# Kernel optimization log

Hardware: AMD Instinct MI355X
Metric: run time of the kernel (lower is better)

Reference implementation:

```python
import jax, jax.numpy as jnp
import numpy as np

ATOM_FDIM = 35
BOND_FDIM = 5
MAX_NB = 15
HIDDEN = 512
DEPTH = 6
N_MOLS = 1024
ATOMS_PER_MOL = 32
N_ATOMS = N_MOLS * ATOMS_PER_MOL      # 32768
N_BONDS = 2 * N_ATOMS                  # 65536 (each bond appears in both directions)
N_MESS = 8192                          # tree messages (row 0 is the zero pad slot)
TOTAL_MSG = N_MESS + N_BONDS           # index space for agraph/bgraph


def setup_inputs() -> dict:
    key = jax.random.key(0)
    ks = jax.random.split(key, 8)
    fatoms = jax.random.normal(ks[0], (N_ATOMS, ATOM_FDIM), jnp.float32)
    fbonds = jax.random.normal(ks[1], (N_BONDS, ATOM_FDIM + BOND_FDIM), jnp.float32)
    agraph = jax.random.randint(ks[2], (N_ATOMS, MAX_NB), 0, TOTAL_MSG, dtype=jnp.int32)
    bgraph = jax.random.randint(ks[3], (N_BONDS, MAX_NB), 0, TOTAL_MSG, dtype=jnp.int32)
    # row 0 of the concatenated message table is the padding slot -> zero it
    tree_message = jax.random.normal(ks[4], (N_MESS, HIDDEN), jnp.float32).at[0].set(0.0)
    starts = jnp.arange(N_MOLS, dtype=jnp.int32) * ATOMS_PER_MOL
    scope = jnp.stack([starts, jnp.full((N_MOLS,), ATOMS_PER_MOL, jnp.int32)], axis=1)
    s_i = 1.0 / np.sqrt(ATOM_FDIM + BOND_FDIM)
    s_h = 1.0 / np.sqrt(HIDDEN)
    s_o = 1.0 / np.sqrt(ATOM_FDIM + HIDDEN)
    W_i = jax.random.normal(ks[5], (ATOM_FDIM + BOND_FDIM, HIDDEN), jnp.float32) * s_i
    W_h = jax.random.normal(ks[6], (HIDDEN, HIDDEN), jnp.float32) * s_h
    W_o = jax.random.normal(ks[7], (ATOM_FDIM + HIDDEN, HIDDEN), jnp.float32) * s_o
    b_o = jnp.zeros((HIDDEN,), jnp.float32)
    return {"fatoms": fatoms, "fbonds": fbonds, "agraph": agraph, "bgraph": bgraph,
            "scope": scope, "tree_message": tree_message,
            "W_i": W_i, "W_h": W_h, "W_o": W_o, "b_o": b_o}


def reference(fatoms, fbonds, agraph, bgraph, scope, tree_message, W_i, W_h, W_o, b_o):
    binput = fbonds @ W_i                         # [B, H]
    graph_message = jax.nn.relu(binput)

    def step(gm, _):
        message = jnp.concatenate([tree_message, gm], axis=0)   # [M+B, H]
        nei = message[bgraph].sum(axis=1)                       # gather-sum [B, H]
        return jax.nn.relu(binput + nei @ W_h), None

    graph_message, _ = jax.lax.scan(step, graph_message, None, length=DEPTH - 1)

    message = jnp.concatenate([tree_message, graph_message], axis=0)
    nei = message[agraph].sum(axis=1)             # [A, H]
    ainput = jnp.concatenate([fatoms, nei], axis=1)
    atom_hiddens = jax.nn.relu(ainput @ W_o + b_o)

    # scope is uniform (st = i*ATOMS_PER_MOL, le = ATOMS_PER_MOL) -> static segment ids
    seg = jnp.repeat(jnp.arange(N_MOLS), ATOMS_PER_MOL)
    sums = jax.ops.segment_sum(atom_hiddens, seg, num_segments=N_MOLS)
    return sums / scope[:, 1:].astype(atom_hiddens.dtype)
```

## Files before the change

### kernel.cpp

```cpp
#include <hip/hip_runtime.h>
#include <stdint.h>


#define MAX_NB 15
#define HID 512
#define NA 32768
#define NB 65536
#define NMESS 8192

typedef unsigned short u16;
typedef unsigned int u32;
typedef __bf16 bf16x8 __attribute__((ext_vector_type(8)));
typedef float f32x4 __attribute__((ext_vector_type(4)));

__device__ __forceinline__ u16 f2bf(float f) {
  u32 u = __builtin_bit_cast(u32, f);
  u32 r = (u + 0x7fffu + ((u >> 16) & 1u)) >> 16;
  return (u16)r;
}
__device__ __forceinline__ float bf2f(u16 b) {
  u32 u = ((u32)b) << 16;
  return __builtin_bit_cast(float, u);
}
__device__ __forceinline__ float bflo(u32 u) {
  return __builtin_bit_cast(float, u << 16);
}
__device__ __forceinline__ float bfhi(u32 u) {
  return __builtin_bit_cast(float, u & 0xffff0000u);
}

__device__ __forceinline__ void async16(const u16* g, u16* l) {
  __builtin_amdgcn_global_load_lds(
      (const __attribute__((address_space(1))) u32*)g,
      (__attribute__((address_space(3))) u32*)l, 16, 0, 0);
}

__global__ __launch_bounds__(256) void prep_kernel(
    const float* __restrict__ fbonds, const float* __restrict__ tree,
    const float* __restrict__ Wi, const float* __restrict__ Wh,
    const float* __restrict__ Wo, u16* __restrict__ tree_bf,
    u16* __restrict__ fbpad, u16* __restrict__ wi_t, u16* __restrict__ wh_t,
    u16* __restrict__ wo_t) {
  int t = blockIdx.x * 256 + threadIdx.x;
  const int N0 = NMESS * HID;
  const int N1 = NB * 64;
  const int N2 = 512 * 64;
  const int N3 = 512 * 512;
  const int N4 = 512 * 576;
  if (t < N0) { tree_bf[t] = f2bf(tree[t]); return; }
  t -= N0;
  if (t < N1) {
    int row = t >> 6, c = t & 63;
    fbpad[t] = (c < 40) ? f2bf(fbonds[row * 40 + c]) : (u16)0;
    return;
  }
  t -= N1;
  if (t < N2) {
    int n = t >> 6, k = t & 63;
    wi_t[t] = (k < 40) ? f2bf(Wi[k * 512 + n]) : (u16)0;
    return;
  }
  t -= N2;
  if (t < N3) {
    int n = t >> 9, k = t & 511;
    wh_t[t] = f2bf(Wh[k * 512 + n]);
    return;
  }
  t -= N3;
  if (t < N4) {
    int n = t / 576, k = t - n * 576;
    float v = 0.f;
    if (k < 512) v = Wo[(35 + k) * 512 + n];
    else if (k < 547) v = Wo[(k - 512) * 512 + n];
    wo_t[t] = f2bf(v);
    return;
  }
}

__global__ __launch_bounds__(256) void init_gemm(
    const u16* __restrict__ A, const u16* __restrict__ Bt,
    u16* __restrict__ binput, u16* __restrict__ gm0) {
  const int K = 64;
  __shared__ __align__(16) u16 As[128 * 32];
  __shared__ __align__(16) u16 Bs[128 * 32];
  const int t = threadIdx.x;
  const int lane = t & 63;
  const int w = t >> 6;
  const int wm = w & 1, wn = w >> 1;
  const int mBase = blockIdx.x * 128;
  const int nBase = blockIdx.y * 128;
  const int r = t >> 2;
  const int c8 = (t & 3) * 8;
  const int q8 = (lane >> 4) * 8;
  const int l15 = lane & 15;

  f32x4 acc[4][4];
#pragma unroll
  for (int i = 0; i < 4; i++)
#pragma unroll
    for (int j = 0; j < 4; j++)
#pragma unroll
      for (int rg = 0; rg < 4; rg++) acc[i][j][rg] = 0.f;

  for (int kb = 0; kb < K; kb += 32) {
    __syncthreads();
    async16(A + (size_t)(mBase + r) * K + kb + c8, As + r * 32 + c8);
    async16(A + (size_t)(mBase + r + 64) * K + kb + c8, As + (r + 64) * 32 + c8);
    async16(Bt + (size_t)(nBase + r) * K + kb + c8, Bs + r * 32 + c8);
    async16(Bt + (size_t)(nBase + r + 64) * K + kb + c8, Bs + (r + 64) * 32 + c8);
    __syncthreads();
    bf16x8 av[4], bv[4];
#pragma unroll
    for (int i = 0; i < 4; i++)
      av[i] = *(const bf16x8*)(As + (wm * 64 + i * 16 + l15) * 32 + q8);
#pragma unroll
    for (int j = 0; j < 4; j++)
      bv[j] = *(const bf16x8*)(Bs + (wn * 64 + j * 16 + l15) * 32 + q8);
#pragma unroll
    for (int i = 0; i < 4; i++)
#pragma unroll
      for (int j = 0; j < 4; j++)
        acc[i][j] = __builtin_amdgcn_mfma_f32_16x16x32_bf16(av[i], bv[j],
                                                            acc[i][j], 0, 0, 0);
  }
#pragma unroll
  for (int i = 0; i < 4; i++) {
    int row = mBase + wm * 64 + i * 16 + (lane >> 4) * 4;
#pragma unroll
    for (int j = 0; j < 4; j++) {
      int col = nBase + wn * 64 + j * 16 + l15;
#pragma unroll
      for (int rg = 0; rg < 4; rg++) {
        float v = acc[i][j][rg];
        size_t gi = (size_t)(row + rg) * HID + col;
        binput[gi] = f2bf(v);
        gm0[gi] = f2bf(fmaxf(v, 0.f));
      }
    }
  }
}

template <int OUT>
__global__ __launch_bounds__(512, 4) void fused_step(
    const u16* __restrict__ tree, const u16* __restrict__ gm_prev,
    const int* __restrict__ graph, const u16* __restrict__ Bt,
    const u16* __restrict__ binput, u16* __restrict__ gm_next,
    const float* __restrict__ fatoms, const float* __restrict__ bo,
    const int* __restrict__ scope, float* __restrict__ out) {
  const int K = OUT ? 576 : 512;
  const int NCH = K / 64;
  __shared__ __align__(16) u16 As[64 * 72];
  const int t = threadIdx.x;
  const int lane = t & 63;
  const int w = t >> 6;
  const int l15 = lane & 15;
  const int q8 = (lane >> 4) * 8;
  const int mBase = blockIdx.x * 64;
  const int slot = t >> 3;
  const int sub = t & 7;

  f32x4 acc[4][4];
#pragma unroll
  for (int i = 0; i < 4; i++)
#pragma unroll
    for (int j = 0; j < 4; j++)
#pragma unroll
      for (int rg = 0; rg < 4; rg++) acc[i][j][rg] = 0.f;

  const int* idx = graph + (size_t)(mBase + slot) * MAX_NB;
  const u16* gm_sh = gm_prev - (size_t)NMESS * HID;

  for (int ch = 0; ch < NCH; ch++) {
    const int kb = ch * 64;
    __syncthreads();
    float g[8] = {0.f, 0.f, 0.f, 0.f, 0.f, 0.f, 0.f, 0.f};
    if (OUT && ch == NCH - 1) {
#pragma unroll
      for (int e = 0; e < 8; e++) {
        int c = sub * 8 + e;
        g[e] = (c < 35) ? fatoms[(size_t)(mBase + slot) * 35 + c] : 0.f;
      }
    } else {
#pragma unroll
      for (int j = 0; j < MAX_NB; j++) {
        int id = idx[j];
        const u16* base = (id < NMESS) ? tree : gm_sh;
        uint4 v = *(const uint4*)(base + (size_t)id * HID + kb + sub * 8);
        g[0] += bflo(v.x); g[1] += bfhi(v.x);
        g[2] += bflo(v.y); g[3] += bfhi(v.y);
        g[4] += bflo(v.z); g[5] += bfhi(v.z);
        g[6] += bflo(v.w); g[7] += bfhi(v.w);
      }
    }
    uint4 o;
    o.x = (u32)f2bf(g[0]) | ((u32)f2bf(g[1]) << 16);
    o.y = (u32)f2bf(g[2]) | ((u32)f2bf(g[3]) << 16);
    o.z = (u32)f2bf(g[4]) | ((u32)f2bf(g[5]) << 16);
    o.w = (u32)f2bf(g[6]) | ((u32)f2bf(g[7]) << 16);
    *(uint4*)(As + slot * 72 + sub * 8) = o;
    __syncthreads();
#pragma unroll
    for (int s = 0; s < 2; s++) {
      bf16x8 av[4], bv[4];
#pragma unroll
      for (int i = 0; i < 4; i++)
        av[i] = *(const bf16x8*)(As + (i * 16 + l15) * 72 + s * 32 + q8);
#pragma unroll
      for (int j = 0; j < 4; j++)
        bv[j] = *(const bf16x8*)(Bt + (size_t)(w * 64 + j * 16 + l15) * K + kb +
                                 s * 32 + q8);
#pragma unroll
      for (int i = 0; i < 4; i++)
#pragma unroll
        for (int j = 0; j < 4; j++)
          acc[i][j] = __builtin_amdgcn_mfma_f32_16x16x32_bf16(
              av[i], bv[j], acc[i][j], 0, 0, 0);
    }
  }

  if (OUT) {
#pragma unroll
    for (int m = 0; m < 2; m++) {
      int mol = (mBase >> 5) + m;
      float inv_le = 1.0f / (float)scope[mol * 2 + 1];
#pragma unroll
      for (int j = 0; j < 4; j++) {
        int col = w * 64 + j * 16 + l15;
        float bias = bo[col];
        float s = 0.f;
#pragma unroll
        for (int i = 2 * m; i < 2 * m + 2; i++)
#pragma unroll
          for (int rg = 0; rg < 4; rg++)
            s += fmaxf(acc[i][j][rg] + bias, 0.f);
        s += __shfl_xor(s, 16, 64);
        s += __shfl_xor(s, 32, 64);
        if (lane < 16) out[(size_t)mol * HID + col] = s * inv_le;
      }
    }
  } else {
#pragma unroll
    for (int i = 0; i < 4; i++) {
      int row = mBase + i * 16 + (lane >> 4) * 4;
#pragma unroll
      for (int j = 0; j < 4; j++) {
        int col = w * 64 + j * 16 + l15;
#pragma unroll
        for (int rg = 0; rg < 4; rg++) {
          size_t gi = (size_t)(row + rg) * HID + col;
          float v = acc[i][j][rg] + bf2f(binput[gi]);
          gm_next[gi] = f2bf(fmaxf(v, 0.f));
        }
      }
    }
  }
}

extern "C" void kernel_launch(void* const* d_in, const int* in_sizes, int n_in,
                              void* d_out, int out_size, void* d_ws,
                              size_t ws_size, hipStream_t stream) {
  const float* fatoms = (const float*)d_in[0];
  const float* fbonds = (const float*)d_in[1];
  const int* agraph = (const int*)d_in[2];
  const int* bgraph = (const int*)d_in[3];
  const int* scope = (const int*)d_in[4];
  const float* tree = (const float*)d_in[5];
  const float* Wi = (const float*)d_in[6];
  const float* Wh = (const float*)d_in[7];
  const float* Wo = (const float*)d_in[8];
  const float* bo = (const float*)d_in[9];
  float* out = (float*)d_out;

  char* ws = (char*)d_ws;
  u16* tree_bf = (u16*)(ws);
  u16* gmA = (u16*)(ws + 8388608ull);
  u16* gmB = (u16*)(ws + 75497472ull);
  u16* binput = (u16*)(ws + 142606336ull);
  u16* wi_t = (u16*)(ws + 209715200ull);
  u16* wh_t = (u16*)(ws + 209780736ull);
  u16* wo_t = (u16*)(ws + 210305024ull);
  u16* fbpad = gmB;

  prep_kernel<<<35072, 256, 0, stream>>>(fbonds, tree, Wi, Wh, Wo, tree_bf,
                                         fbpad, wi_t, wh_t, wo_t);

  init_gemm<<<dim3(NB / 128, 4), 256, 0, stream>>>(fbpad, wi_t, binput, gmA);

  u16* prev = gmA;
  u16* next = gmB;
  for (int d = 0; d < 5; d++) {
    fused_step<0><<<NB / 64, 512, 0, stream>>>(tree_bf, prev, bgraph, wh_t,
                                               binput, next, nullptr, nullptr,
                                               nullptr, nullptr);
    u16* tmp = prev; prev = next; next = tmp;
  }

  fused_step<1><<<NA / 64, 512, 0, stream>>>(tree_bf, prev, agraph, wo_t,
                                             nullptr, nullptr, fatoms, bo,
                                             scope, out);
}
```

Before: 1.335 ms.

## Gather full neighbor-sum rows into LDS once, then run the whole K loop

```diff
diff --git a/kernel.cpp b/kernel.cpp
--- a/kernel.cpp
+++ b/kernel.cpp
@@ -141,81 +141,72 @@
 }
 
 template <int OUT>
-__global__ __launch_bounds__(512, 4) void fused_step(
+__global__ __launch_bounds__(512, 4) void fused_mp(
     const u16* __restrict__ tree, const u16* __restrict__ gm_prev,
     const int* __restrict__ graph, const u16* __restrict__ Bt,
     const u16* __restrict__ binput, u16* __restrict__ gm_next,
     const float* __restrict__ fatoms, const float* __restrict__ bo,
     const int* __restrict__ scope, float* __restrict__ out) {
-  const int K = OUT ? 576 : 512;
-  const int NCH = K / 64;
-  __shared__ __align__(16) u16 As[64 * 72];
+  constexpr int K = OUT ? 576 : 512;
+  constexpr int LDA = K + 8;
+  __shared__ __align__(16) u16 As[64 * LDA];
   const int t = threadIdx.x;
   const int lane = t & 63;
   const int w = t >> 6;
+  const int mBase = blockIdx.x * 64;
+  const u16* gm_sh = gm_prev - (size_t)NMESS * HID;
+
+  for (int rr = 0; rr < 8; rr++) {
+    const int row = mBase + w * 8 + rr;
+    const int* idxp = graph + row * MAX_NB;
+    float acc[8] = {0, 0, 0, 0, 0, 0, 0, 0};
+#pragma unroll
+    for (int j = 0; j < MAX_NB; j++) {
+      int id = idxp[j];
+      const u16* base = (id < NMESS) ? tree : gm_sh;
+      uint4 v = *(const uint4*)(base + (size_t)id * HID + lane * 8);
+      acc[0] += bflo(v.x); acc[1] += bfhi(v.x);
+      acc[2] += bflo(v.y); acc[3] += bfhi(v.y);
+      acc[4] += bflo(v.z); acc[5] += bfhi(v.z);
+      acc[6] += bflo(v.w); acc[7] += bfhi(v.w);
+    }
+    uint4 o;
+    o.x = (u32)f2bf(acc[0]) | ((u32)f2bf(acc[1]) << 16);
+    o.y = (u32)f2bf(acc[2]) | ((u32)f2bf(acc[3]) << 16);
+    o.z = (u32)f2bf(acc[4]) | ((u32)f2bf(acc[5]) << 16);
+    o.w = (u32)f2bf(acc[6]) | ((u32)f2bf(acc[7]) << 16);
+    *(uint4*)(As + (w * 8 + rr) * LDA + lane * 8) = o;
+    if (OUT) {
+      float tv = (lane < 35) ? fatoms[(size_t)row * 35 + lane] : 0.f;
+      As[(w * 8 + rr) * LDA + 512 + lane] = f2bf(tv);
+    }
+  }
+  __syncthreads();
+
   const int l15 = lane & 15;
   const int q8 = (lane >> 4) * 8;
-  const int mBase = blockIdx.x * 64;
-  const int slot = t >> 3;
-  const int sub = t & 7;
-
-  f32x4 acc[4][4];
+  f32x4 acc2[4][4];
 #pragma unroll
   for (int i = 0; i < 4; i++)
 #pragma unroll
     for (int j = 0; j < 4; j++)
 #pragma unroll
-      for (int rg = 0; rg < 4; rg++) acc[i][j][rg] = 0.f;
-
-  const int* idx = graph + (size_t)(mBase + slot) * MAX_NB;
-  const u16* gm_sh = gm_prev - (size_t)NMESS * HID;
-
-  for (int ch = 0; ch < NCH; ch++) {
-    const int kb = ch * 64;
-    __syncthreads();
-    float g[8] = {0.f, 0.f, 0.f, 0.f, 0.f, 0.f, 0.f, 0.f};
-    if (OUT && ch == NCH - 1) {
-#pragma unroll
-      for (int e = 0; e < 8; e++) {
-        int c = sub * 8 + e;
-        g[e] = (c < 35) ? fatoms[(size_t)(mBase + slot) * 35 + c] : 0.f;
-      }
-    } else {
-#pragma unroll
-      for (int j = 0; j < MAX_NB; j++) {
-        int id = idx[j];
-        const u16* base = (id < NMESS) ? tree : gm_sh;
-        uint4 v = *(const uint4*)(base + (size_t)id * HID + kb + sub * 8);
-        g[0] += bflo(v.x); g[1] += bfhi(v.x);
-        g[2] += bflo(v.y); g[3] += bfhi(v.y);
-        g[4] += bflo(v.z); g[5] += bfhi(v.z);
-        g[6] += bflo(v.w); g[7] += bfhi(v.w);
-      }
-    }
-    uint4 o;
-    o.x = (u32)f2bf(g[0]) | ((u32)f2bf(g[1]) << 16);
-    o.y = (u32)f2bf(g[2]) | ((u32)f2bf(g[3]) << 16);
-    o.z = (u32)f2bf(g[4]) | ((u32)f2bf(g[5]) << 16);
-    o.w = (u32)f2bf(g[6]) | ((u32)f2bf(g[7]) << 16);
-    *(uint4*)(As + slot * 72 + sub * 8) = o;
-    __syncthreads();
-#pragma unroll
-    for (int s = 0; s < 2; s++) {
-      bf16x8 av[4], bv[4];
-#pragma unroll
-      for (int i = 0; i < 4; i++)
-        av[i] = *(const bf16x8*)(As + (i * 16 + l15) * 72 + s * 32 + q8);
+      for (int rg = 0; rg < 4; rg++) acc2[i][j][rg] = 0.f;
+
+  for (int kb = 0; kb < K; kb += 32) {
+    bf16x8 av[4], bv[4];
+#pragma unroll
+    for (int i = 0; i < 4; i++)
+      av[i] = *(const bf16x8*)(As + (i * 16 + l15) * LDA + kb + q8);
+#pragma unroll
+    for (int j = 0; j < 4; j++)
+      bv[j] = *(const bf16x8*)(Bt + (size_t)(w * 64 + j * 16 + l15) * K + kb + q8);
+#pragma unroll
+    for (int i = 0; i < 4; i++)
 #pragma unroll
       for (int j = 0; j < 4; j++)
-        bv[j] = *(const bf16x8*)(Bt + (size_t)(w * 64 + j * 16 + l15) * K + kb +
-                                 s * 32 + q8);
-#pragma unroll
-      for (int i = 0; i < 4; i++)
-#pragma unroll
-        for (int j = 0; j < 4; j++)
-          acc[i][j] = __builtin_amdgcn_mfma_f32_16x16x32_bf16(
-              av[i], bv[j], acc[i][j], 0, 0, 0);
-    }
+        acc2[i][j] = __builtin_amdgcn_mfma_f32_16x16x32_bf16(av[i], bv[j],
+                                                             acc2[i][j], 0, 0, 0);
   }
 
   if (OUT) {
@@ -232,7 +223,7 @@
         for (int i = 2 * m; i < 2 * m + 2; i++)
 #pragma unroll
           for (int rg = 0; rg < 4; rg++)
-            s += fmaxf(acc[i][j][rg] + bias, 0.f);
+            s += fmaxf(acc2[i][j][rg] + bias, 0.f);
         s += __shfl_xor(s, 16, 64);
         s += __shfl_xor(s, 32, 64);
         if (lane < 16) out[(size_t)mol * HID + col] = s * inv_le;
@@ -248,7 +239,7 @@
 #pragma unroll
         for (int rg = 0; rg < 4; rg++) {
           size_t gi = (size_t)(row + rg) * HID + col;
-          float v = acc[i][j][rg] + bf2f(binput[gi]);
+          float v = acc2[i][j][rg] + bf2f(binput[gi]);
           gm_next[gi] = f2bf(fmaxf(v, 0.f));
         }
       }
@@ -289,13 +280,13 @@
   u16* prev = gmA;
   u16* next = gmB;
   for (int d = 0; d < 5; d++) {
-    fused_step<0><<<NB / 64, 512, 0, stream>>>(tree_bf, prev, bgraph, wh_t,
-                                               binput, next, nullptr, nullptr,
-                                               nullptr, nullptr);
+    fused_mp<0><<<NB / 64, 512, 0, stream>>>(tree_bf, prev, bgraph, wh_t,
+                                             binput, next, nullptr, nullptr,
+                                             nullptr, nullptr);
     u16* tmp = prev; prev = next; next = tmp;
   }
 
-  fused_step<1><<<NA / 64, 512, 0, stream>>>(tree_bf, prev, agraph, wo_t,
-                                             nullptr, nullptr, fatoms, bo,
-                                             scope, out);
-}
+  fused_mp<1><<<NA / 64, 512, 0, stream>>>(tree_bf, prev, agraph, wo_t,
+                                           nullptr, nullptr, fatoms, bo,
+                                           scope, out);
+}
```

Measured after the change: 1.328 ms. About the same (-0.5%).
